# Optimization experiments

Measured on AMD Instinct MI355X. Metric: run time of the kernel, lower is better.

## Reference

```python
import jax, jax.numpy as jnp
import numpy as np

N_HEAD = 16
N_KV = 4
N_EMBD = 2048
HEAD_DIM = N_EMBD // N_HEAD  # 128
GROUP = N_HEAD // N_KV       # 4 queries per kv head


def setup_inputs() -> dict:
    key = jax.random.key(0)
    ks = jax.random.split(key, 5)
    B, S = 2, 2048
    scale = 0.02
    return {
        "x": jax.random.normal(ks[0], (B, S, N_EMBD), dtype=jnp.float32),
        "Wq": jax.random.normal(ks[1], (N_EMBD, N_EMBD), dtype=jnp.float32) * scale,
        "Wk": jax.random.normal(ks[2], (N_EMBD, N_EMBD // GROUP), dtype=jnp.float32) * scale,
        "Wv": jax.random.normal(ks[3], (N_EMBD, N_EMBD // GROUP), dtype=jnp.float32) * scale,
        "Wo": jax.random.normal(ks[4], (N_EMBD, N_EMBD), dtype=jnp.float32) * scale,
    }


def reference(x, Wq, Wk, Wv, Wo):
    B, S, _ = x.shape
    scale = HEAD_DIM ** -0.5
    # projections (bias=False)
    q = (x @ Wq).reshape(B, S, N_KV, GROUP, HEAD_DIM)   # grouped query heads
    k = (x @ Wk).reshape(B, S, N_KV, HEAD_DIM)
    v = (x @ Wv).reshape(B, S, N_KV, HEAD_DIM)
    # scores: repeat_interleave of K over GROUP == broadcast over g axis
    scores = jnp.einsum('bqkgd,bskd->bkgqs', q, k) * scale  # [B,n_kv,g,S,S]
    causal = jnp.triu(jnp.ones((S, S), dtype=bool), k=1)
    scores = jnp.where(causal, jnp.finfo(scores.dtype).min, scores)
    attn = jax.nn.softmax(scores, axis=-1)
    out = jnp.einsum('bkgqs,bskd->bqkgd', attn, v)  # [B,S,n_kv,g,hd]
    out = out.reshape(B, S, N_EMBD)
    return out @ Wo
```

## Files before the change

### kernel.cpp

```cpp
#include <hip/hip_runtime.h>

typedef unsigned short u16;
typedef unsigned int u32;
typedef __attribute__((ext_vector_type(8))) __bf16 bh8;
typedef __attribute__((ext_vector_type(4))) float fx4;

#define AS1 __attribute__((address_space(1)))
#define AS3 __attribute__((address_space(3)))

__device__ __forceinline__ void gll16(const void* g, void* l) {
  void* gg = const_cast<void*>(g);
  __builtin_amdgcn_global_load_lds((AS1 void*)gg, (AS3 void*)l, 16, 0, 0);
}

__device__ __forceinline__ u16 f2b(float f) {
  union { float f; u32 u; } v; v.f = f;
  u32 r = v.u + 0x7FFFu + ((v.u >> 16) & 1u);
  return (u16)(r >> 16);
}

__device__ __forceinline__ fx4 fzero() { fx4 z = {0.f, 0.f, 0.f, 0.f}; return z; }

#define MFMA16(a, b, c) __builtin_amdgcn_mfma_f32_16x16x32_bf16(a, b, c, 0, 0, 0)

__global__ void k_cast(const float* __restrict__ in, u16* __restrict__ out, int n4) {
  int i = blockIdx.x * blockDim.x + threadIdx.x;
  if (i >= n4) return;
  float4 v = reinterpret_cast<const float4*>(in)[i];
  ushort4 o;
  o.x = f2b(v.x); o.y = f2b(v.y); o.z = f2b(v.z); o.w = f2b(v.w);
  reinterpret_cast<ushort4*>(out)[i] = o;
}

__global__ void k_transpose_cast(const float* __restrict__ in, u16* __restrict__ out,
                                 int R, int C) {
  __shared__ float t[32][33];
  int tx = threadIdx.x, ty = threadIdx.y;
  int r0 = blockIdx.y * 32, c0 = blockIdx.x * 32;
#pragma unroll
  for (int j = 0; j < 4; j++)
    t[ty + 8 * j][tx] = in[(size_t)(r0 + ty + 8 * j) * C + c0 + tx];
  __syncthreads();
#pragma unroll
  for (int j = 0; j < 4; j++)
    out[(size_t)(c0 + ty + 8 * j) * R + r0 + tx] = f2b(t[tx][ty + 8 * j]);
}

__global__ void k_transpose_v(const u16* __restrict__ in, u16* __restrict__ out) {
  __shared__ u16 t[32][33];
  int tx = threadIdx.x, ty = threadIdx.y;
  int s0 = blockIdx.x * 32, d0 = blockIdx.y * 32;
  int z = blockIdx.z, b = z >> 2, kv = z & 3;
#pragma unroll
  for (int j = 0; j < 4; j++)
    t[ty + 8 * j][tx] = in[(size_t)(b * 2048 + s0 + ty + 8 * j) * 512 + kv * 128 + d0 + tx];
  __syncthreads();
#pragma unroll
  for (int j = 0; j < 4; j++)
    out[(size_t)(z * 128 + d0 + ty + 8 * j) * 2048 + s0 + tx] = t[tx][ty + 8 * j];
}

__device__ __forceinline__ void gemm_core(const u16* __restrict__ A, const u16* __restrict__ Bt,
                                          int bm, int bn, u16* As, u16* Bs, fx4 acc[4][4]) {
  const int tid = threadIdx.x;
  const int lane = tid & 63, w = tid >> 6;
  const int wr = w >> 1, wc = w & 1;
  const int i = lane & 15, g = lane >> 4;
  const int c0 = tid, c1 = tid + 256;
  const u16* ga0 = A + (size_t)(bm + (c0 >> 2)) * 2048 + (c0 & 3) * 8;
  const u16* ga1 = A + (size_t)(bm + (c1 >> 2)) * 2048 + (c1 & 3) * 8;
  const u16* gb0 = Bt + (size_t)(bn + (c0 >> 2)) * 2048 + (c0 & 3) * 8;
  const u16* gb1 = Bt + (size_t)(bn + (c1 >> 2)) * 2048 + (c1 & 3) * 8;
  u16* la0 = As + c0 * 8; u16* la1 = As + c1 * 8;
  u16* lb0 = Bs + c0 * 8; u16* lb1 = Bs + c1 * 8;
  const u16* ra = As + (wr * 64 + i) * 32 + g * 8;
  const u16* rb = Bs + (wc * 64 + i) * 32 + g * 8;
  for (int kt = 0; kt < 2048; kt += 32) {
    __syncthreads();
    gll16(ga0 + kt, la0);
    gll16(ga1 + kt, la1);
    gll16(gb0 + kt, lb0);
    gll16(gb1 + kt, lb1);
    __syncthreads();
    bh8 af[4], bfr[4];
#pragma unroll
    for (int m = 0; m < 4; m++) af[m] = *reinterpret_cast<const bh8*>(ra + m * 16 * 32);
#pragma unroll
    for (int n = 0; n < 4; n++) bfr[n] = *reinterpret_cast<const bh8*>(rb + n * 16 * 32);
#pragma unroll
    for (int m = 0; m < 4; m++)
#pragma unroll
      for (int n = 0; n < 4; n++)
        acc[m][n] = MFMA16(af[m], bfr[n], acc[m][n]);
  }
}

__global__ __launch_bounds__(256, 2) void k_proj(const u16* __restrict__ xb,
                                                 const u16* __restrict__ Wqt,
                                                 const u16* __restrict__ Wkt,
                                                 const u16* __restrict__ Wvt,
                                                 u16* __restrict__ Qb, u16* __restrict__ Kb,
                                                 u16* __restrict__ Vb) {
  __shared__ __align__(16) u16 As[128 * 32];
  __shared__ __align__(16) u16 Bs[128 * 32];
  int by = blockIdx.y;
  const u16* Bt; u16* Cp; int bn, ldc; float alpha;
  if (by < 16)      { Bt = Wqt; Cp = Qb; bn = by * 128;        ldc = 2048; alpha = 0.08838834764831845f; }
  else if (by < 20) { Bt = Wkt; Cp = Kb; bn = (by - 16) * 128; ldc = 512;  alpha = 1.0f; }
  else              { Bt = Wvt; Cp = Vb; bn = (by - 20) * 128; ldc = 512;  alpha = 1.0f; }
  int bm = blockIdx.x * 128;
  fx4 acc[4][4];
#pragma unroll
  for (int m = 0; m < 4; m++)
#pragma unroll
    for (int n = 0; n < 4; n++) acc[m][n] = fzero();
  gemm_core(xb, Bt, bm, bn, As, Bs, acc);
  const int lane = threadIdx.x & 63, w = threadIdx.x >> 6;
  const int wr = w >> 1, wc = w & 1, i = lane & 15, g = lane >> 4;
#pragma unroll
  for (int m = 0; m < 4; m++)
#pragma unroll
    for (int n = 0; n < 4; n++)
#pragma unroll
      for (int r = 0; r < 4; r++) {
        int row = bm + wr * 64 + m * 16 + 4 * g + r;
        int col = bn + wc * 64 + n * 16 + i;
        Cp[(size_t)row * ldc + col] = f2b(acc[m][n][r] * alpha);
      }
}

__global__ __launch_bounds__(256, 2) void k_gemm_out(const u16* __restrict__ Ob,
                                                     const u16* __restrict__ Wot,
                                                     float* __restrict__ C) {
  __shared__ __align__(16) u16 As[128 * 32];
  __shared__ __align__(16) u16 Bs[128 * 32];
  int bm = blockIdx.x * 128, bn = blockIdx.y * 128;
  fx4 acc[4][4];
#pragma unroll
  for (int m = 0; m < 4; m++)
#pragma unroll
    for (int n = 0; n < 4; n++) acc[m][n] = fzero();
  gemm_core(Ob, Wot, bm, bn, As, Bs, acc);
  const int lane = threadIdx.x & 63, w = threadIdx.x >> 6;
  const int wr = w >> 1, wc = w & 1, i = lane & 15, g = lane >> 4;
#pragma unroll
  for (int m = 0; m < 4; m++)
#pragma unroll
    for (int n = 0; n < 4; n++)
#pragma unroll
      for (int r = 0; r < 4; r++) {
        int row = bm + wr * 64 + m * 16 + 4 * g + r;
        int col = bn + wc * 64 + n * 16 + i;
        C[(size_t)row * 2048 + col] = acc[m][n][r];
      }
}

__global__ __launch_bounds__(256, 2) void k_attn(const u16* __restrict__ Qb,
                                                 const u16* __restrict__ Kb,
                                                 const u16* __restrict__ Vt,
                                                 u16* __restrict__ Ob) {
  __shared__ __align__(16) u16 Ks[64 * 128];
  __shared__ __align__(16) u16 Vs[128 * 64];
  __shared__ __align__(16) u16 Pl[4][16 * 72];
  const int tid = threadIdx.x, lane = tid & 63, w = tid >> 6;
  const int i = lane & 15, g = lane >> 4;
  const int qb = blockIdx.x * 64;
  const int head = blockIdx.y, b = blockIdx.z, kv = head >> 2;
  const int qmin = qb + w * 16;

  const u16* qptr = Qb + (size_t)(b * 2048 + qmin + i) * 2048 + head * 128 + g * 8;
  bh8 qf[4];
#pragma unroll
  for (int kb = 0; kb < 4; kb++) qf[kb] = *reinterpret_cast<const bh8*>(qptr + kb * 32);

  fx4 o[8];
#pragma unroll
  for (int dt = 0; dt < 8; dt++) o[dt] = fzero();
  float m[4] = {-1e30f, -1e30f, -1e30f, -1e30f};
  float l[4] = {0.f, 0.f, 0.f, 0.f};

  for (int s0 = 0; s0 < qb + 64; s0 += 64) {
    __syncthreads();
#pragma unroll
    for (int cc = 0; cc < 4; cc++) {
      int c = tid + cc * 256;
      gll16(Kb + (size_t)(b * 2048 + s0 + (c >> 4)) * 512 + kv * 128 +
                (((c & 15) ^ ((c >> 4) & 7)) * 8),
            Ks + c * 8);
      gll16(Vt + (size_t)((b * 4 + kv) * 128 + (c >> 3)) * 2048 + s0 +
                (((c & 7) ^ ((c >> 3) & 7)) * 8),
            Vs + c * 8);
    }
    __syncthreads();

    fx4 sc[4];
#pragma unroll
    for (int st = 0; st < 4; st++) {
      sc[st] = fzero();
#pragma unroll
      for (int kb = 0; kb < 4; kb++) {
        bh8 kf = *reinterpret_cast<const bh8*>(Ks + (st * 16 + i) * 128 +
                                               (((kb * 4 + g) ^ (i & 7)) * 8));
        sc[st] = MFMA16(qf[kb], kf, sc[st]);
      }
    }

    if (s0 + 63 > qmin) {
#pragma unroll
      for (int st = 0; st < 4; st++)
#pragma unroll
        for (int r = 0; r < 4; r++) {
          int s = s0 + st * 16 + i;
          int q = qmin + 4 * g + r;
          if (s > q) sc[st][r] = -1e30f;
        }
    }

    float corr[4];
#pragma unroll
    for (int r = 0; r < 4; r++) {
      float v = fmaxf(fmaxf(sc[0][r], sc[1][r]), fmaxf(sc[2][r], sc[3][r]));
      v = fmaxf(v, __shfl_xor(v, 1));
      v = fmaxf(v, __shfl_xor(v, 2));
      v = fmaxf(v, __shfl_xor(v, 4));
      v = fmaxf(v, __shfl_xor(v, 8));
      float mn = fmaxf(m[r], v);
      corr[r] = __expf(m[r] - mn);
      m[r] = mn;
    }
    float p[4][4];
#pragma unroll
    for (int r = 0; r < 4; r++) {
      float s = 0.f;
#pragma unroll
      for (int st = 0; st < 4; st++) { p[st][r] = __expf(sc[st][r] - m[r]); s += p[st][r]; }
      s += __shfl_xor(s, 1); s += __shfl_xor(s, 2);
      s += __shfl_xor(s, 4); s += __shfl_xor(s, 8);
      l[r] = l[r] * corr[r] + s;
    }
#pragma unroll
    for (int dt = 0; dt < 8; dt++)
#pragma unroll
      for (int r = 0; r < 4; r++) o[dt][r] *= corr[r];

#pragma unroll
    for (int st = 0; st < 4; st++)
#pragma unroll
      for (int r = 0; r < 4; r++)
        Pl[w][(4 * g + r) * 72 + st * 16 + i] = f2b(p[st][r]);

    bh8 pf0 = *reinterpret_cast<const bh8*>(&Pl[w][i * 72 + g * 8]);
    bh8 pf1 = *reinterpret_cast<const bh8*>(&Pl[w][i * 72 + 32 + g * 8]);
#pragma unroll
    for (int dt = 0; dt < 8; dt++) {
      bh8 v0 = *reinterpret_cast<const bh8*>(Vs + (dt * 16 + i) * 64 + (((g) ^ (i & 7)) * 8));
      bh8 v1 = *reinterpret_cast<const bh8*>(Vs + (dt * 16 + i) * 64 + (((4 + g) ^ (i & 7)) * 8));
      o[dt] = MFMA16(pf0, v0, o[dt]);
      o[dt] = MFMA16(pf1, v1, o[dt]);
    }
  }

#pragma unroll
  for (int r = 0; r < 4; r++) {
    float inv = 1.0f / l[r];
#pragma unroll
    for (int dt = 0; dt < 8; dt++)
      Ob[(size_t)(b * 2048 + qmin + 4 * g + r) * 2048 + head * 128 + dt * 16 + i] =
          f2b(o[dt][r] * inv);
  }
}

extern "C" void kernel_launch(void* const* d_in, const int* in_sizes, int n_in,
                              void* d_out, int out_size, void* d_ws, size_t ws_size,
                              hipStream_t stream) {
  (void)in_sizes; (void)n_in; (void)out_size; (void)ws_size;
  const float* x  = (const float*)d_in[0];
  const float* Wq = (const float*)d_in[1];
  const float* Wk = (const float*)d_in[2];
  const float* Wv = (const float*)d_in[3];
  const float* Wo = (const float*)d_in[4];

  char* ws = (char*)d_ws;
  size_t off = 0;
  auto alloc = [&](size_t bytes) {
    void* p = ws + off;
    off += (bytes + 255) & ~(size_t)255;
    return p;
  };
  u16* xb  = (u16*)alloc(8388608ull * 2);
  u16* Wqt = (u16*)alloc(4194304ull * 2);
  u16* Wkt = (u16*)alloc(1048576ull * 2);
  u16* Wvt = (u16*)alloc(1048576ull * 2);
  u16* Wot = (u16*)alloc(4194304ull * 2);
  u16* Qb  = (u16*)alloc(8388608ull * 2);
  u16* Kb  = (u16*)alloc(2097152ull * 2);
  u16* Vb  = (u16*)alloc(2097152ull * 2);
  u16* Vt  = (u16*)alloc(2097152ull * 2);
  u16* Ob  = xb;

  k_cast<<<8192, 256, 0, stream>>>(x, xb, 2097152);
  k_transpose_cast<<<dim3(64, 64), dim3(32, 8), 0, stream>>>(Wq, Wqt, 2048, 2048);
  k_transpose_cast<<<dim3(16, 64), dim3(32, 8), 0, stream>>>(Wk, Wkt, 2048, 512);
  k_transpose_cast<<<dim3(16, 64), dim3(32, 8), 0, stream>>>(Wv, Wvt, 2048, 512);
  k_transpose_cast<<<dim3(64, 64), dim3(32, 8), 0, stream>>>(Wo, Wot, 2048, 2048);
  k_proj<<<dim3(32, 24), 256, 0, stream>>>(xb, Wqt, Wkt, Wvt, Qb, Kb, Vb);
  k_transpose_v<<<dim3(64, 4, 8), dim3(32, 8), 0, stream>>>(Vb, Vt);
  k_attn<<<dim3(32, 16, 2), 256, 0, stream>>>(Qb, Kb, Vt, Ob);
  k_gemm_out<<<dim3(32, 16), 256, 0, stream>>>(Ob, Wot, (float*)d_out);
}
```

Baseline: 371.8 us.

## Pair causal query tiles per block and double-buffer K/V staging

Each attention block now handles two query tiles, j and 31-j, so every block does the same amount of causal work, and the grid is halved. Both tiles share each staged K/V tile, and K/V loads are double-buffered so the next tile's global-to-LDS copy overlaps the current tile's compute. The P scratch buffer drops its padding in favour of an XOR swizzle to avoid bank conflicts. In exchange, register pressure roughly doubles (two sets of accumulators and Q fragments), LDS use grows, and the grid has only 512 blocks, which may reduce occupancy.

```diff
diff --git a/kernel.cpp b/kernel.cpp
--- a/kernel.cpp
+++ b/kernel.cpp
@@ -159,52 +159,70 @@
                                                  const u16* __restrict__ Kb,
                                                  const u16* __restrict__ Vt,
                                                  u16* __restrict__ Ob) {
-  __shared__ __align__(16) u16 Ks[64 * 128];
-  __shared__ __align__(16) u16 Vs[128 * 64];
-  __shared__ __align__(16) u16 Pl[4][16 * 72];
+  __shared__ __align__(16) u16 Ks[2][64 * 128];
+  __shared__ __align__(16) u16 Vs[2][128 * 64];
+  __shared__ __align__(16) u16 Pl[4][16 * 64];
   const int tid = threadIdx.x, lane = tid & 63, w = tid >> 6;
   const int i = lane & 15, g = lane >> 4;
-  const int qb = blockIdx.x * 64;
+  const int j = blockIdx.x;
   const int head = blockIdx.y, b = blockIdx.z, kv = head >> 2;
-  const int qmin = qb + w * 16;
-
-  const u16* qptr = Qb + (size_t)(b * 2048 + qmin + i) * 2048 + head * 128 + g * 8;
-  bh8 qf[4];
-#pragma unroll
-  for (int kb = 0; kb < 4; kb++) qf[kb] = *reinterpret_cast<const bh8*>(qptr + kb * 32);
-
-  fx4 o[8];
-#pragma unroll
-  for (int dt = 0; dt < 8; dt++) o[dt] = fzero();
-  float m[4] = {-1e30f, -1e30f, -1e30f, -1e30f};
-  float l[4] = {0.f, 0.f, 0.f, 0.f};
-
-  for (int s0 = 0; s0 < qb + 64; s0 += 64) {
-    __syncthreads();
+  const int qa = j, qc = 31 - j;
+  const int qmin_a = qa * 64 + w * 16, qmin_c = qc * 64 + w * 16;
+  const int nt = 32 - j;
+  const int nta = j + 1;
+
+  const u16* kbase[4];
+  const u16* vbase[4];
+  u16* kdst[2][4];
+  u16* vdst[2][4];
+#pragma unroll
+  for (int cc = 0; cc < 4; cc++) {
+    int c = tid + cc * 256;
+    kbase[cc] = Kb + (size_t)(b * 2048 + (c >> 4)) * 512 + kv * 128 +
+                (((c & 15) ^ ((c >> 4) & 7)) * 8);
+    vbase[cc] = Vt + (size_t)((b * 4 + kv) * 128 + (c >> 3)) * 2048 +
+                (((c & 7) ^ ((c >> 3) & 7)) * 8);
+    kdst[0][cc] = Ks[0] + c * 8; kdst[1][cc] = Ks[1] + c * 8;
+    vdst[0][cc] = Vs[0] + c * 8; vdst[1][cc] = Vs[1] + c * 8;
+  }
+
+  bh8 qfa[4], qfc[4];
+  {
+    const u16* qpa = Qb + (size_t)(b * 2048 + qmin_a + i) * 2048 + head * 128 + g * 8;
+    const u16* qpc = Qb + (size_t)(b * 2048 + qmin_c + i) * 2048 + head * 128 + g * 8;
+#pragma unroll
+    for (int kb = 0; kb < 4; kb++) {
+      qfa[kb] = *reinterpret_cast<const bh8*>(qpa + kb * 32);
+      qfc[kb] = *reinterpret_cast<const bh8*>(qpc + kb * 32);
+    }
+  }
+
+  fx4 oa[8], oc[8];
+#pragma unroll
+  for (int dt = 0; dt < 8; dt++) { oa[dt] = fzero(); oc[dt] = fzero(); }
+  float ma[4] = {-1e30f, -1e30f, -1e30f, -1e30f}, la[4] = {0.f, 0.f, 0.f, 0.f};
+  float mc[4] = {-1e30f, -1e30f, -1e30f, -1e30f}, lc[4] = {0.f, 0.f, 0.f, 0.f};
+
+  auto STAGE = [&](int buf, int s0) {
 #pragma unroll
     for (int cc = 0; cc < 4; cc++) {
-      int c = tid + cc * 256;
-      gll16(Kb + (size_t)(b * 2048 + s0 + (c >> 4)) * 512 + kv * 128 +
-                (((c & 15) ^ ((c >> 4) & 7)) * 8),
-            Ks + c * 8);
-      gll16(Vt + (size_t)((b * 4 + kv) * 128 + (c >> 3)) * 2048 + s0 +
-                (((c & 7) ^ ((c >> 3) & 7)) * 8),
-            Vs + c * 8);
-    }
-    __syncthreads();
-
+      gll16(kbase[cc] + (size_t)s0 * 512, kdst[buf][cc]);
+      gll16(vbase[cc] + s0, vdst[buf][cc]);
+    }
+  };
+
+  auto TILE = [&](const bh8* qf, fx4* o, float* m, float* l, int qmin, int buf, int s0) {
     fx4 sc[4];
 #pragma unroll
     for (int st = 0; st < 4; st++) {
       sc[st] = fzero();
 #pragma unroll
       for (int kb = 0; kb < 4; kb++) {
-        bh8 kf = *reinterpret_cast<const bh8*>(Ks + (st * 16 + i) * 128 +
+        bh8 kf = *reinterpret_cast<const bh8*>(Ks[buf] + (st * 16 + i) * 128 +
                                                (((kb * 4 + g) ^ (i & 7)) * 8));
         sc[st] = MFMA16(qf[kb], kf, sc[st]);
       }
     }
-
     if (s0 + 63 > qmin) {
 #pragma unroll
       for (int st = 0; st < 4; st++)
@@ -215,7 +233,6 @@
           if (s > q) sc[st][r] = -1e30f;
         }
     }
-
     float corr[4];
 #pragma unroll
     for (int r = 0; r < 4; r++) {
@@ -246,27 +263,47 @@
 #pragma unroll
     for (int st = 0; st < 4; st++)
 #pragma unroll
-      for (int r = 0; r < 4; r++)
-        Pl[w][(4 * g + r) * 72 + st * 16 + i] = f2b(p[st][r]);
-
-    bh8 pf0 = *reinterpret_cast<const bh8*>(&Pl[w][i * 72 + g * 8]);
-    bh8 pf1 = *reinterpret_cast<const bh8*>(&Pl[w][i * 72 + 32 + g * 8]);
+      for (int r = 0; r < 4; r++) {
+        int row = 4 * g + r;
+        int cg = st * 2 + (i >> 3);
+        Pl[w][row * 64 + ((cg ^ (row & 7)) << 3) + (i & 7)] = f2b(p[st][r]);
+      }
+    bh8 pf0 = *reinterpret_cast<const bh8*>(&Pl[w][i * 64 + ((g ^ (i & 7)) << 3)]);
+    bh8 pf1 = *reinterpret_cast<const bh8*>(&Pl[w][i * 64 + (((4 + g) ^ (i & 7)) << 3)]);
 #pragma unroll
     for (int dt = 0; dt < 8; dt++) {
-      bh8 v0 = *reinterpret_cast<const bh8*>(Vs + (dt * 16 + i) * 64 + (((g) ^ (i & 7)) * 8));
-      bh8 v1 = *reinterpret_cast<const bh8*>(Vs + (dt * 16 + i) * 64 + (((4 + g) ^ (i & 7)) * 8));
+      bh8 v0 = *reinterpret_cast<const bh8*>(Vs[buf] + (dt * 16 + i) * 64 +
+                                             ((g ^ (i & 7)) * 8));
+      bh8 v1 = *reinterpret_cast<const bh8*>(Vs[buf] + (dt * 16 + i) * 64 +
+                                             (((4 + g) ^ (i & 7)) * 8));
       o[dt] = MFMA16(pf0, v0, o[dt]);
       o[dt] = MFMA16(pf1, v1, o[dt]);
     }
+  };
+
+  int cur = 0;
+  STAGE(0, 0);
+  __syncthreads();
+  for (int t = 0; t < nt; t++) {
+    int s0 = t * 64;
+    if (t + 1 < nt) STAGE(cur ^ 1, s0 + 64);
+    TILE(qfc, oc, mc, lc, qmin_c, cur, s0);
+    if (t < nta) TILE(qfa, oa, ma, la, qmin_a, cur, s0);
+    __syncthreads();
+    cur ^= 1;
   }
 
 #pragma unroll
   for (int r = 0; r < 4; r++) {
-    float inv = 1.0f / l[r];
-#pragma unroll
-    for (int dt = 0; dt < 8; dt++)
-      Ob[(size_t)(b * 2048 + qmin + 4 * g + r) * 2048 + head * 128 + dt * 16 + i] =
-          f2b(o[dt][r] * inv);
+    float inva = 1.0f / la[r];
+    float invc = 1.0f / lc[r];
+#pragma unroll
+    for (int dt = 0; dt < 8; dt++) {
+      Ob[(size_t)(b * 2048 + qmin_a + 4 * g + r) * 2048 + head * 128 + dt * 16 + i] =
+          f2b(oa[dt][r] * inva);
+      Ob[(size_t)(b * 2048 + qmin_c + 4 * g + r) * 2048 + head * 128 + dt * 16 + i] =
+          f2b(oc[dt][r] * invc);
+    }
   }
 }
 
@@ -305,6 +342,6 @@
   k_transpose_cast<<<dim3(64, 64), dim3(32, 8), 0, stream>>>(Wo, Wot, 2048, 2048);
   k_proj<<<dim3(32, 24), 256, 0, stream>>>(xb, Wqt, Wkt, Wvt, Qb, Kb, Vb);
   k_transpose_v<<<dim3(64, 4, 8), dim3(32, 8), 0, stream>>>(Vb, Vt);
-  k_attn<<<dim3(32, 16, 2), 256, 0, stream>>>(Qb, Kb, Vt, Ob);
+  k_attn<<<dim3(16, 16, 2), 256, 0, stream>>>(Qb, Kb, Vt, Ob);
   k_gemm_out<<<dim3(32, 16), 256, 0, stream>>>(Ob, Wot, (float*)d_out);
 }
```

Result: slower. 552.0 us (+48.5%).
